# Optimization experiments

Measured on AMD Instinct MI355X. Metric: run time of the kernel, lower is better.

## Reference

```python
import jax, jax.numpy as jnp
import numpy as np

D_IN = 256
DIMS = 256


def setup_inputs() -> dict:
    key = jax.random.key(0)
    k1, k2, k3, k4, k5 = jax.random.split(key, 5)
    B, Tq, Tk = 4, 512, 512
    query = jax.random.normal(k1, (B, Tq, D_IN), dtype=jnp.float32)
    value = jax.random.normal(k2, (B, Tk, D_IN), dtype=jnp.float32)
    # Dense(dims, use_bias=False) kernels (glorot-like scale) and AdditiveAttention scale vector
    Wq = jax.random.normal(k3, (D_IN, DIMS), dtype=jnp.float32) / np.sqrt(D_IN)
    Wv = jax.random.normal(k4, (D_IN, DIMS), dtype=jnp.float32) / np.sqrt(D_IN)
    scale = jax.random.normal(k5, (DIMS,), dtype=jnp.float32)
    return {"query": query, "value": value, "Wq": Wq, "Wv": Wv, "scale": scale}


def reference(query, value, Wq, Wv, scale):
    # q_proj: [B,Tq,d], k_proj: [B,Tk,d]; attention value = RAW value tensor (as in source)
    q = jnp.einsum("bqi,id->bqd", query, Wq)
    k = jnp.einsum("bki,id->bkd", value, Wv)
    # Additive (Bahdanau) scores: [B,Tq,Tk] via broadcast tanh then reduce with scale
    scores = jnp.einsum("bqkd,d->bqk", jnp.tanh(q[:, :, None, :] + k[:, None, :, :]), scale)
    attn = jax.nn.softmax(scores, axis=-1)  # masks are all-ones -> no-op
    out = jnp.einsum("bqk,bki->bqi", attn, value)
    return out, attn
```

## Files before the change

kernel.cpp:

```cpp
#include <hip/hip_runtime.h>

#define LOG2E 1.4426950408889634f
#define TWO_LOG2E 2.885390081777927f

__device__ __forceinline__ float fast_exp2(float x) { return __builtin_amdgcn_exp2f(x); }
__device__ __forceinline__ float fast_rcp(float x)  { return __builtin_amdgcn_rcpf(x); }

__device__ __forceinline__ void term2(float s0, float s1, float qx, float qy,
                                      float kx, float ky, float& acc) {
    const float A = fmaf(qx, kx, 1.f);
    const float B = fmaf(qy, ky, 1.f);
    acc = fmaf(fmaf(s1, A, s0 * B), fast_rcp(A * B), acc);
}

__global__ __launch_bounds__(256) void proj_kernel(
    const float* __restrict__ query, const float* __restrict__ value,
    const float* __restrict__ Wq, const float* __restrict__ Wv,
    float* __restrict__ eq, float* __restrict__ ekT)
{
    __shared__ float in_lds[8 * 256];
    const int t = threadIdx.x;
    const int row0 = blockIdx.x * 8;
    const float* src; const float* W;
    if (row0 < 2048) { src = query + (size_t)row0 * 256; W = Wq; }
    else { src = value + (size_t)(row0 - 2048) * 256; W = Wv; }

    const float4* s4 = (const float4*)src;
    float4* l4 = (float4*)in_lds;
    l4[t] = s4[t];
    l4[t + 256] = s4[t + 256];
    __syncthreads();

    float acc[8];
#pragma unroll
    for (int r = 0; r < 8; ++r) acc[r] = 0.f;

    for (int d = 0; d < 256; d += 4) {
        const float w0 = W[(d + 0) * 256 + t];
        const float w1 = W[(d + 1) * 256 + t];
        const float w2 = W[(d + 2) * 256 + t];
        const float w3 = W[(d + 3) * 256 + t];
#pragma unroll
        for (int r = 0; r < 8; ++r) {
            const float4 v = *(const float4*)&in_lds[r * 256 + d];
            acc[r] = fmaf(v.x, w0, acc[r]);
            acc[r] = fmaf(v.y, w1, acc[r]);
            acc[r] = fmaf(v.z, w2, acc[r]);
            acc[r] = fmaf(v.w, w3, acc[r]);
        }
    }

    if (row0 < 2048) {
        float* dst = eq + (size_t)row0 * 256;
#pragma unroll
        for (int r = 0; r < 8; ++r) dst[r * 256 + t] = fast_exp2(acc[r] * TWO_LOG2E);
    } else {
        const int r0 = row0 - 2048;
        const int bb = r0 >> 9, kin = r0 & 511;
        float* dstT = ekT + (size_t)bb * 131072 + (size_t)t * 512 + kin;
        float4 v0, v1;
        v0.x = fast_exp2(acc[0] * TWO_LOG2E); v0.y = fast_exp2(acc[1] * TWO_LOG2E);
        v0.z = fast_exp2(acc[2] * TWO_LOG2E); v0.w = fast_exp2(acc[3] * TWO_LOG2E);
        v1.x = fast_exp2(acc[4] * TWO_LOG2E); v1.y = fast_exp2(acc[5] * TWO_LOG2E);
        v1.z = fast_exp2(acc[6] * TWO_LOG2E); v1.w = fast_exp2(acc[7] * TWO_LOG2E);
        *(float4*)dstT = v0;
        *(float4*)(dstT + 4) = v1;
    }
}

#define EQ_ST 260
#define SS_ST 520
__global__ __launch_bounds__(512, 2) void fused_kernel(
    const float* __restrict__ eq, const float* __restrict__ ekT,
    const float* __restrict__ scale, const float* __restrict__ value,
    float* __restrict__ attn, float* __restrict__ out)
{
    __shared__ float eq_lds[8 * EQ_ST];
    __shared__ float sc_lds[256];
    __shared__ float s_tile[8 * SS_ST];
    __shared__ float red[4 * 8 * 256];
    __shared__ float inv_lds[8];

    const int t = threadIdx.x;
    const int w = t >> 6, lane = t & 63;
    const int qg = w >> 2;
    const int kg = ((w & 3) << 6) + lane;
    const int k0 = 2 * kg;
    const int qt = blockIdx.x, b = blockIdx.y;
    const int q0 = qt * 8;

    {
        const int row = t >> 6, c = t & 63;
        const float4 v = ((const float4*)(eq + (size_t)(b * 512 + q0) * 256))[row * 64 + c];
        *(float4*)&eq_lds[row * EQ_ST + 4 * c] = v;
    }
    if (t < 256) sc_lds[t] = -2.f * scale[t];
    __syncthreads();

    const float* ekTb = ekT + (size_t)b * 131072 + k0;
    const float* q0r = &eq_lds[(4 * qg + 0) * EQ_ST];
    const float* q1r = &eq_lds[(4 * qg + 1) * EQ_ST];
    const float* q2r = &eq_lds[(4 * qg + 2) * EQ_ST];
    const float* q3r = &eq_lds[(4 * qg + 3) * EQ_ST];

    float a00 = 0.f, a01 = 0.f, a10 = 0.f, a11 = 0.f;
    float a20 = 0.f, a21 = 0.f, a30 = 0.f, a31 = 0.f;

    float4 svA  = *(const float4*)&sc_lds[0];
    float4 qv0A = *(const float4*)&q0r[0];
    float4 qv1A = *(const float4*)&q1r[0];
    float4 qv2A = *(const float4*)&q2r[0];
    float4 qv3A = *(const float4*)&q3r[0];
    float2 k0A = *(const float2*)&ekTb[(size_t)0 * 512];
    float2 k1A = *(const float2*)&ekTb[(size_t)1 * 512];
    float2 k2A = *(const float2*)&ekTb[(size_t)2 * 512];
    float2 k3A = *(const float2*)&ekTb[(size_t)3 * 512];

    float4 svB  = *(const float4*)&sc_lds[4];
    float4 qv0B = *(const float4*)&q0r[4];
    float4 qv1B = *(const float4*)&q1r[4];
    float4 qv2B = *(const float4*)&q2r[4];
    float4 qv3B = *(const float4*)&q3r[4];
    float2 k0B = *(const float2*)&ekTb[(size_t)4 * 512];
    float2 k1B = *(const float2*)&ekTb[(size_t)5 * 512];
    float2 k2B = *(const float2*)&ekTb[(size_t)6 * 512];
    float2 k3B = *(const float2*)&ekTb[(size_t)7 * 512];

#pragma unroll 2
    for (int d = 0; d < 256; d += 8) {
        {
            const float4 csv = svA, c0 = qv0A, c1 = qv1A, c2 = qv2A, c3 = qv3A;
            const float2 ck0 = k0A, ck1 = k1A, ck2 = k2A, ck3 = k3A;
            if (d < 248) {
                const int dn = d + 8;
                svA  = *(const float4*)&sc_lds[dn];
                qv0A = *(const float4*)&q0r[dn];
                qv1A = *(const float4*)&q1r[dn];
                qv2A = *(const float4*)&q2r[dn];
                qv3A = *(const float4*)&q3r[dn];
                k0A = *(const float2*)&ekTb[(size_t)(dn + 0) * 512];
                k1A = *(const float2*)&ekTb[(size_t)(dn + 1) * 512];
                k2A = *(const float2*)&ekTb[(size_t)(dn + 2) * 512];
                k3A = *(const float2*)&ekTb[(size_t)(dn + 3) * 512];
            }
            term2(csv.x, csv.y, c0.x, c0.y, ck0.x, ck1.x, a00);
            term2(csv.z, csv.w, c0.z, c0.w, ck2.x, ck3.x, a00);
            term2(csv.x, csv.y, c0.x, c0.y, ck0.y, ck1.y, a01);
            term2(csv.z, csv.w, c0.z, c0.w, ck2.y, ck3.y, a01);
            term2(csv.x, csv.y, c1.x, c1.y, ck0.x, ck1.x, a10);
            term2(csv.z, csv.w, c1.z, c1.w, ck2.x, ck3.x, a10);
            term2(csv.x, csv.y, c1.x, c1.y, ck0.y, ck1.y, a11);
            term2(csv.z, csv.w, c1.z, c1.w, ck2.y, ck3.y, a11);
            term2(csv.x, csv.y, c2.x, c2.y, ck0.x, ck1.x, a20);
            term2(csv.z, csv.w, c2.z, c2.w, ck2.x, ck3.x, a20);
            term2(csv.x, csv.y, c2.x, c2.y, ck0.y, ck1.y, a21);
            term2(csv.z, csv.w, c2.z, c2.w, ck2.y, ck3.y, a21);
            term2(csv.x, csv.y, c3.x, c3.y, ck0.x, ck1.x, a30);
            term2(csv.z, csv.w, c3.z, c3.w, ck2.x, ck3.x, a30);
            term2(csv.x, csv.y, c3.x, c3.y, ck0.y, ck1.y, a31);
            term2(csv.z, csv.w, c3.z, c3.w, ck2.y, ck3.y, a31);
        }
        {
            const float4 csv = svB, c0 = qv0B, c1 = qv1B, c2 = qv2B, c3 = qv3B;
            const float2 ck0 = k0B, ck1 = k1B, ck2 = k2B, ck3 = k3B;
            if (d < 244) {
                const int dn = d + 12;
                svB  = *(const float4*)&sc_lds[dn];
                qv0B = *(const float4*)&q0r[dn];
                qv1B = *(const float4*)&q1r[dn];
                qv2B = *(const float4*)&q2r[dn];
                qv3B = *(const float4*)&q3r[dn];
                k0B = *(const float2*)&ekTb[(size_t)(dn + 0) * 512];
                k1B = *(const float2*)&ekTb[(size_t)(dn + 1) * 512];
                k2B = *(const float2*)&ekTb[(size_t)(dn + 2) * 512];
                k3B = *(const float2*)&ekTb[(size_t)(dn + 3) * 512];
            }
            term2(csv.x, csv.y, c0.x, c0.y, ck0.x, ck1.x, a00);
            term2(csv.z, csv.w, c0.z, c0.w, ck2.x, ck3.x, a00);
            term2(csv.x, csv.y, c0.x, c0.y, ck0.y, ck1.y, a01);
            term2(csv.z, csv.w, c0.z, c0.w, ck2.y, ck3.y, a01);
            term2(csv.x, csv.y, c1.x, c1.y, ck0.x, ck1.x, a10);
            term2(csv.z, csv.w, c1.z, c1.w, ck2.x, ck3.x, a10);
            term2(csv.x, csv.y, c1.x, c1.y, ck0.y, ck1.y, a11);
            term2(csv.z, csv.w, c1.z, c1.w, ck2.y, ck3.y, a11);
            term2(csv.x, csv.y, c2.x, c2.y, ck0.x, ck1.x, a20);
            term2(csv.z, csv.w, c2.z, c2.w, ck2.x, ck3.x, a20);
            term2(csv.x, csv.y, c2.x, c2.y, ck0.y, ck1.y, a21);
            term2(csv.z, csv.w, c2.z, c2.w, ck2.y, ck3.y, a21);
            term2(csv.x, csv.y, c3.x, c3.y, ck0.x, ck1.x, a30);
            term2(csv.z, csv.w, c3.z, c3.w, ck2.x, ck3.x, a30);
            term2(csv.x, csv.y, c3.x, c3.y, ck0.y, ck1.y, a31);
            term2(csv.z, csv.w, c3.z, c3.w, ck2.y, ck3.y, a31);
        }
    }

    *(float2*)&s_tile[(4 * qg + 0) * SS_ST + k0] = make_float2(a00, a01);
    *(float2*)&s_tile[(4 * qg + 1) * SS_ST + k0] = make_float2(a10, a11);
    *(float2*)&s_tile[(4 * qg + 2) * SS_ST + k0] = make_float2(a20, a21);
    *(float2*)&s_tile[(4 * qg + 3) * SS_ST + k0] = make_float2(a30, a31);
    __syncthreads();

    {
        float x[8];
        float m = -1e30f;
#pragma unroll
        for (int j = 0; j < 8; ++j) {
            x[j] = s_tile[w * SS_ST + 64 * j + lane];
            m = fmaxf(m, x[j]);
        }
#pragma unroll
        for (int off = 32; off; off >>= 1) m = fmaxf(m, __shfl_xor(m, off));

        float sum = 0.f;
#pragma unroll
        for (int j = 0; j < 8; ++j) { x[j] = fast_exp2((x[j] - m) * LOG2E); sum += x[j]; }
#pragma unroll
        for (int off = 32; off; off >>= 1) sum += __shfl_xor(sum, off);
        const float inv = fast_rcp(sum);

        float* arow = attn + (size_t)(b * 512 + q0 + w) * 512;
#pragma unroll
        for (int j = 0; j < 8; ++j) {
            s_tile[w * SS_ST + 64 * j + lane] = x[j];
            arow[64 * j + lane] = x[j] * inv;
        }
        if (lane == 0) inv_lds[w] = inv;
    }
    __syncthreads();

    float4 acc[8];
#pragma unroll
    for (int r = 0; r < 8; ++r) acc[r] = make_float4(0.f, 0.f, 0.f, 0.f);

    const float* vbase = value + (size_t)(b * 512 + 64 * w) * 256;
    for (int k4 = 0; k4 < 64; k4 += 4) {
        const float4 v0 = *(const float4*)&vbase[(k4 + 0) * 256 + lane * 4];
        const float4 v1 = *(const float4*)&vbase[(k4 + 1) * 256 + lane * 4];
        const float4 v2 = *(const float4*)&vbase[(k4 + 2) * 256 + lane * 4];
        const float4 v3 = *(const float4*)&vbase[(k4 + 3) * 256 + lane * 4];
#pragma unroll
        for (int r = 0; r < 8; ++r) {
            const float4 s4 = *(const float4*)&s_tile[r * SS_ST + 64 * w + k4];
            acc[r].x = fmaf(s4.x, v0.x, acc[r].x); acc[r].y = fmaf(s4.x, v0.y, acc[r].y);
            acc[r].z = fmaf(s4.x, v0.z, acc[r].z); acc[r].w = fmaf(s4.x, v0.w, acc[r].w);
            acc[r].x = fmaf(s4.y, v1.x, acc[r].x); acc[r].y = fmaf(s4.y, v1.y, acc[r].y);
            acc[r].z = fmaf(s4.y, v1.z, acc[r].z); acc[r].w = fmaf(s4.y, v1.w, acc[r].w);
            acc[r].x = fmaf(s4.z, v2.x, acc[r].x); acc[r].y = fmaf(s4.z, v2.y, acc[r].y);
            acc[r].z = fmaf(s4.z, v2.z, acc[r].z); acc[r].w = fmaf(s4.z, v2.w, acc[r].w);
            acc[r].x = fmaf(s4.w, v3.x, acc[r].x); acc[r].y = fmaf(s4.w, v3.y, acc[r].y);
            acc[r].z = fmaf(s4.w, v3.z, acc[r].z); acc[r].w = fmaf(s4.w, v3.w, acc[r].w);
        }
    }

    if (w >= 4) {
#pragma unroll
        for (int r = 0; r < 8; ++r)
            *(float4*)&red[((w - 4) * 8 + r) * 256 + lane * 4] = acc[r];
    }
    __syncthreads();
    if (w < 4) {
#pragma unroll
        for (int r = 0; r < 8; ++r) {
            const float4 o = *(const float4*)&red[(w * 8 + r) * 256 + lane * 4];
            acc[r].x += o.x; acc[r].y += o.y; acc[r].z += o.z; acc[r].w += o.w;
        }
    }
    __syncthreads();
    if (w >= 2 && w < 4) {
#pragma unroll
        for (int r = 0; r < 8; ++r)
            *(float4*)&red[((w - 2) * 8 + r) * 256 + lane * 4] = acc[r];
    }
    __syncthreads();
    if (w < 2) {
#pragma unroll
        for (int r = 0; r < 8; ++r) {
            const float4 o = *(const float4*)&red[(w * 8 + r) * 256 + lane * 4];
            acc[r].x += o.x; acc[r].y += o.y; acc[r].z += o.z; acc[r].w += o.w;
        }
    }
    __syncthreads();
    if (w == 1) {
#pragma unroll
        for (int r = 0; r < 8; ++r)
            *(float4*)&red[r * 256 + lane * 4] = acc[r];
    }
    __syncthreads();
    if (w == 0) {
#pragma unroll
        for (int r = 0; r < 8; ++r) {
            const float4 o = *(const float4*)&red[r * 256 + lane * 4];
            const float iv = inv_lds[r];
            float4 res;
            res.x = (acc[r].x + o.x) * iv;
            res.y = (acc[r].y + o.y) * iv;
            res.z = (acc[r].z + o.z) * iv;
            res.w = (acc[r].w + o.w) * iv;
            *(float4*)&out[(size_t)(b * 512 + q0 + r) * 256 + lane * 4] = res;
        }
    }
}

extern "C" void kernel_launch(void* const* d_in, const int* in_sizes, int n_in,
                              void* d_out, int out_size, void* d_ws, size_t ws_size,
                              hipStream_t stream) {
    const float* query = (const float*)d_in[0];
    const float* value = (const float*)d_in[1];
    const float* Wq    = (const float*)d_in[2];
    const float* Wv    = (const float*)d_in[3];
    const float* scale = (const float*)d_in[4];

    float* out0 = (float*)d_out;
    float* attn = out0 + 4 * 512 * 256;

    float* eq  = (float*)d_ws;
    float* ekT = eq + 2048 * 256;

    proj_kernel<<<512, 256, 0, stream>>>(query, value, Wq, Wv, eq, ekT);
    fused_kernel<<<dim3(64, 4), 512, 0, stream>>>(eq, ekT, scale, value, attn, out0);
}
```

Measured before the change: 63.86 us.

## Tile value projection through LDS and transpose for coalesced ekT stores

The value half of the projection kernel becomes a 64-key by 32-output register-blocked tile. Value and Wv chunks are staged in padded LDS, and the exp results are transposed through LDS so they can be written to ekT as coalesced float4 rows. Previously each thread wrote 8 values at a stride of 512 floats, so the stores were scattered, and every block reloaded Wv from global memory. The query path is unchanged and the grid size stays the same. The cost is extra LDS and barriers in a kernel that is likely a minor share of total time.

```diff
diff --git a/kernel.cpp b/kernel.cpp
--- a/kernel.cpp
+++ b/kernel.cpp
@@ -19,52 +19,104 @@
     float* __restrict__ eq, float* __restrict__ ekT)
 {
     __shared__ float in_lds[8 * 256];
+    __shared__ float v_lds[64 * 68];
+    __shared__ float w_lds[64 * 36];
+    __shared__ float t_lds[32 * 68];
+
     const int t = threadIdx.x;
-    const int row0 = blockIdx.x * 8;
-    const float* src; const float* W;
-    if (row0 < 2048) { src = query + (size_t)row0 * 256; W = Wq; }
-    else { src = value + (size_t)(row0 - 2048) * 256; W = Wv; }
-
-    const float4* s4 = (const float4*)src;
-    float4* l4 = (float4*)in_lds;
-    l4[t] = s4[t];
-    l4[t + 256] = s4[t + 256];
-    __syncthreads();
-
-    float acc[8];
-#pragma unroll
-    for (int r = 0; r < 8; ++r) acc[r] = 0.f;
-
-    for (int d = 0; d < 256; d += 4) {
-        const float w0 = W[(d + 0) * 256 + t];
-        const float w1 = W[(d + 1) * 256 + t];
-        const float w2 = W[(d + 2) * 256 + t];
-        const float w3 = W[(d + 3) * 256 + t];
-#pragma unroll
-        for (int r = 0; r < 8; ++r) {
-            const float4 v = *(const float4*)&in_lds[r * 256 + d];
-            acc[r] = fmaf(v.x, w0, acc[r]);
-            acc[r] = fmaf(v.y, w1, acc[r]);
-            acc[r] = fmaf(v.z, w2, acc[r]);
-            acc[r] = fmaf(v.w, w3, acc[r]);
-        }
-    }
-
-    if (row0 < 2048) {
+    const int bx = blockIdx.x;
+
+    if (bx < 256) {
+        const int row0 = bx * 8;
+        const float4* s4 = (const float4*)(query + (size_t)row0 * 256);
+        float4* l4 = (float4*)in_lds;
+        l4[t] = s4[t];
+        l4[t + 256] = s4[t + 256];
+        __syncthreads();
+
+        float acc[8];
+#pragma unroll
+        for (int r = 0; r < 8; ++r) acc[r] = 0.f;
+
+        for (int d = 0; d < 256; d += 4) {
+            const float w0 = Wq[(d + 0) * 256 + t];
+            const float w1 = Wq[(d + 1) * 256 + t];
+            const float w2 = Wq[(d + 2) * 256 + t];
+            const float w3 = Wq[(d + 3) * 256 + t];
+#pragma unroll
+            for (int r = 0; r < 8; ++r) {
+                const float4 v = *(const float4*)&in_lds[r * 256 + d];
+                acc[r] = fmaf(v.x, w0, acc[r]);
+                acc[r] = fmaf(v.y, w1, acc[r]);
+                acc[r] = fmaf(v.z, w2, acc[r]);
+                acc[r] = fmaf(v.w, w3, acc[r]);
+            }
+        }
         float* dst = eq + (size_t)row0 * 256;
 #pragma unroll
         for (int r = 0; r < 8; ++r) dst[r * 256 + t] = fast_exp2(acc[r] * TWO_LOG2E);
     } else {
-        const int r0 = row0 - 2048;
-        const int bb = r0 >> 9, kin = r0 & 511;
-        float* dstT = ekT + (size_t)bb * 131072 + (size_t)t * 512 + kin;
-        float4 v0, v1;
-        v0.x = fast_exp2(acc[0] * TWO_LOG2E); v0.y = fast_exp2(acc[1] * TWO_LOG2E);
-        v0.z = fast_exp2(acc[2] * TWO_LOG2E); v0.w = fast_exp2(acc[3] * TWO_LOG2E);
-        v1.x = fast_exp2(acc[4] * TWO_LOG2E); v1.y = fast_exp2(acc[5] * TWO_LOG2E);
-        v1.z = fast_exp2(acc[6] * TWO_LOG2E); v1.w = fast_exp2(acc[7] * TWO_LOG2E);
-        *(float4*)dstT = v0;
-        *(float4*)(dstT + 4) = v1;
+        const int bi = bx - 256;
+        const int kt = bi >> 3, dt = bi & 7;
+        const int gk0 = kt * 64;
+        const int bb = gk0 >> 9, kin0 = gk0 & 511;
+        const int dout0 = dt * 32;
+        const int kp = t >> 3, dg = t & 7;
+
+        float acc[2][4];
+#pragma unroll
+        for (int i = 0; i < 2; ++i)
+#pragma unroll
+            for (int j = 0; j < 4; ++j) acc[i][j] = 0.f;
+
+        for (int dc = 0; dc < 256; dc += 64) {
+            __syncthreads();
+#pragma unroll
+            for (int l = 0; l < 4; ++l) {
+                const int idx = t + 256 * l;
+                const int r = idx >> 4, c4 = (idx & 15) * 4;
+                *(float4*)&v_lds[r * 68 + c4] =
+                    *(const float4*)&value[(size_t)(gk0 + r) * 256 + dc + c4];
+            }
+#pragma unroll
+            for (int l = 0; l < 2; ++l) {
+                const int idx = t + 256 * l;
+                const int r = idx >> 3, c4 = (idx & 7) * 4;
+                *(float4*)&w_lds[r * 36 + c4] =
+                    *(const float4*)&Wv[(size_t)(dc + r) * 256 + dout0 + c4];
+            }
+            __syncthreads();
+
+#pragma unroll 8
+            for (int din = 0; din < 64; ++din) {
+                const float v0 = v_lds[(2 * kp + 0) * 68 + din];
+                const float v1 = v_lds[(2 * kp + 1) * 68 + din];
+                const float4 wv = *(const float4*)&w_lds[din * 36 + 4 * dg];
+                acc[0][0] = fmaf(v0, wv.x, acc[0][0]);
+                acc[0][1] = fmaf(v0, wv.y, acc[0][1]);
+                acc[0][2] = fmaf(v0, wv.z, acc[0][2]);
+                acc[0][3] = fmaf(v0, wv.w, acc[0][3]);
+                acc[1][0] = fmaf(v1, wv.x, acc[1][0]);
+                acc[1][1] = fmaf(v1, wv.y, acc[1][1]);
+                acc[1][2] = fmaf(v1, wv.z, acc[1][2]);
+                acc[1][3] = fmaf(v1, wv.w, acc[1][3]);
+            }
+        }
+        __syncthreads();
+#pragma unroll
+        for (int i = 0; i < 2; ++i)
+#pragma unroll
+            for (int j = 0; j < 4; ++j)
+                t_lds[(4 * dg + j) * 68 + 2 * kp + i] =
+                    fast_exp2(acc[i][j] * TWO_LOG2E);
+        __syncthreads();
+#pragma unroll
+        for (int l = 0; l < 2; ++l) {
+            const int idx = t + 256 * l;
+            const int row = idx >> 4, c4 = (idx & 15) * 4;
+            *(float4*)&ekT[(size_t)bb * 131072 + (size_t)(dout0 + row) * 512 + kin0 + c4] =
+                *(const float4*)&t_lds[row * 68 + c4];
+        }
     }
 }
 
```

New measurement: 61.52 us, median of 2. -3.7%, faster.
